# Performance work log

Hardware: AMD Instinct MI355X
Metric: run time of the kernel (lower is better)

Reference implementation:

```python
import jax, jax.numpy as jnp
import numpy as np

B, S, D, NH = 8, 2048, 1024, 8
HD = D // NH          # 128 head dim
UP = 2752             # round_up(2.6667*1024, 64) gated FFN up dim
EPS = 1e-6


def setup_inputs() -> dict:
    key = jax.random.key(0)
    ks = jax.random.split(key, 10)
    s_hd = 1.0 / np.sqrt(HD)
    s_d = 1.0 / np.sqrt(D)
    s_up = 1.0 / np.sqrt(UP)
    return {
        "x": jax.random.normal(ks[0], (B, S, D), jnp.float32),
        "rms1_w": 1.0 + 0.1 * jax.random.normal(ks[1], (D,), jnp.float32),
        "rms2_w": 1.0 + 0.1 * jax.random.normal(ks[2], (D,), jnp.float32),
        # block-diagonal per-head input projections for the 4 gates (i,f,z,o)
        "Wg": jax.random.normal(ks[3], (4, NH, HD, HD), jnp.float32) * s_hd,
        # block-diagonal per-head recurrent weights for the 4 gates
        "R": jax.random.normal(ks[4], (4, NH, HD, HD), jnp.float32) * s_hd,
        "b": jax.random.normal(ks[5], (4, D), jnp.float32) * 0.1,
        "gn_w": 1.0 + 0.1 * jax.random.normal(ks[6], (D,), jnp.float32),
        "W_gate": jax.random.normal(ks[7], (D, UP), jnp.float32) * s_d,
        "W_up": jax.random.normal(ks[8], (D, UP), jnp.float32) * s_d,
        "W_down": jax.random.normal(ks[9], (UP, D), jnp.float32) * s_up,
    }


def _rmsnorm(x, w):
    xf = x.astype(jnp.float32)
    return xf * jax.lax.rsqrt(jnp.mean(xf * xf, axis=-1, keepdims=True) + EPS) * w


def _slstm_block(x, rms1_w, rms2_w, Wg, R, b, gn_w, W_gate, W_up, W_down):
    # --- norm + sLSTM layer ---
    xn = _rmsnorm(x, rms1_w)                     # [B,S,D]
    xh = xn.reshape(B, S, NH, HD)
    # precompute input-side gate preactivations for all timesteps: [S,B,4,NH,HD]
    gx = jnp.einsum('bsni,gnoi->sbgno', xh, Wg) + b.reshape(4, NH, HD)

    zeros = jnp.zeros((B, NH, HD), jnp.float32)
    init = (zeros, zeros, zeros, zeros)          # h, c, n, m

    def step(carry, g):
        h, c, n, m = carry
        pre = g + jnp.einsum('bni,gnoi->bgno', h, R)   # [B,4,NH,HD]
        ir, fr, zr, o_r = pre[:, 0], pre[:, 1], pre[:, 2], pre[:, 3]
        logfplusm = m + jax.nn.log_sigmoid(fr)
        mnew = jnp.maximum(ir, logfplusm)
        i = jnp.exp(ir - mnew)
        f = jnp.exp(logfplusm - mnew)
        cnew = f * c + i * jnp.tanh(zr)
        nnew = f * n + i
        hnew = jax.nn.sigmoid(o_r) * cnew / nnew
        return (hnew, cnew, nnew, mnew), hnew

    (hl, cl, nl, ml), hs = jax.lax.scan(step, init, gx)
    hs = jnp.transpose(hs, (1, 0, 2, 3))         # [B,S,NH,HD]
    # per-head group norm (zero-mean layernorm within each head), weight only
    mu = jnp.mean(hs, axis=-1, keepdims=True)
    var = jnp.var(hs, axis=-1, keepdims=True)
    y = ((hs - mu) * jax.lax.rsqrt(var + EPS)).reshape(B, S, D) * gn_w
    x = x + y                                    # residual
    # --- norm + gated SiLU FFN ---
    xn2 = _rmsnorm(x, rms2_w)
    ff = (jax.nn.silu(xn2 @ W_gate) * (xn2 @ W_up)) @ W_down
    out = x + ff
    state = jnp.stack([hl, cl, nl, ml])          # [4,B,NH,HD] last (h,c,n,m)
    return out, state


def reference(x, rms1_w, rms2_w, Wg, R, b, gn_w, W_gate, W_up, W_down):
    return _slstm_block(x, rms1_w, rms2_w, Wg, R, b, gn_w, W_gate, W_up, W_down)
```

## Files before the change

### kernel.cpp

```cpp
#include <hip/hip_runtime.h>

typedef __bf16 bf16;
typedef bf16 bf16x8 __attribute__((ext_vector_type(8)));
typedef bf16 bf16x4 __attribute__((ext_vector_type(4)));
typedef float f32x4 __attribute__((ext_vector_type(4)));

#define B_ 8
#define S_ 2048
#define D_ 1024
#define NH_ 8
#define HD_ 128
#define UPP 2816
#define ROWS (B_*S_)

__device__ __forceinline__ void gload_lds16(const void* gsrc, void* ldsdst) {
  __builtin_amdgcn_global_load_lds(
      (const __attribute__((address_space(1))) void*)gsrc,
      (__attribute__((address_space(3))) void*)ldsdst, 16, 0, 0);
}

__global__ __launch_bounds__(256) void pack_wgr_kernel(
    const float* __restrict__ Wg, const float* __restrict__ R, const float* __restrict__ bv,
    bf16* __restrict__ Wgpk, bf16* __restrict__ Rpk, float* __restrict__ biaspk)
{
  const float K2 = 1.442695040888963f;
  int idx = blockIdx.x * 256 + threadIdx.x;
  if (idx < 8*512*128) {
    int k = idx & 127, j = (idx >> 7) & 511, n = idx >> 16;
    int g = (j >> 4) & 3, o = ((j >> 6) << 4) | (j & 15);
    float sc = (g == 2) ? 2.f*K2 : K2;
    size_t src = (((size_t)(g*8 + n)*128 + o)*128 + k);
    Wgpk[idx] = (bf16)(Wg[src] * sc);
    Rpk[idx]  = (bf16)(R[src] * sc);
  }
  if (idx < 8*512) {
    int j = idx & 511, n = idx >> 9;
    int g = (j >> 4) & 3, o = ((j >> 6) << 4) | (j & 15);
    float sc = (g == 2) ? 2.f*K2 : K2;
    biaspk[idx] = bv[g*1024 + n*128 + o] * sc;
  }
}

__global__ __launch_bounds__(256) void packT_kernel(
    const float* __restrict__ in, bf16* __restrict__ out,
    int K_out, int N_out, int K_in, int N_in)
{
  __shared__ float tile[64][65];
  int k0 = blockIdx.x * 64, j0 = blockIdx.y * 64;
  int tj = threadIdx.x & 63, t4 = threadIdx.x >> 6;
  #pragma unroll
  for (int p = 0; p < 16; ++p) {
    int kk = p*4 + t4, k = k0 + kk, j = j0 + tj;
    tile[kk][tj] = (k < K_in && j < N_in) ? in[(size_t)k * N_in + j] : 0.f;
  }
  __syncthreads();
  #pragma unroll
  for (int p = 0; p < 16; ++p) {
    int jj = p*4 + t4, j = j0 + jj, k = k0 + tj;
    if (j < N_out && k < K_out) out[(size_t)j * K_out + k] = (bf16)tile[tj][jj];
  }
}

__global__ __launch_bounds__(256) void rmsnorm1_kernel(
    const float* __restrict__ x, const float* __restrict__ w, bf16* __restrict__ xn)
{
  const int row = blockIdx.x, t = threadIdx.x;
  const size_t base = (size_t)row * D_;
  float4 xv = ((const float4*)(x + base))[t];
  float p = xv.x*xv.x + xv.y*xv.y + xv.z*xv.z + xv.w*xv.w;
  #pragma unroll
  for (int m = 1; m <= 32; m <<= 1) p += __shfl_xor(p, m);
  __shared__ float red[4];
  if ((t & 63) == 0) red[t >> 6] = p;
  __syncthreads();
  float rs = rsqrtf((red[0]+red[1]+red[2]+red[3]) * (1.f/1024.f) + 1e-6f);
  float4 wv = ((const float4*)w)[t];
  bf16x4 o;
  o[0] = (bf16)(xv.x*rs*wv.x); o[1] = (bf16)(xv.y*rs*wv.y);
  o[2] = (bf16)(xv.z*rs*wv.z); o[3] = (bf16)(xv.w*rs*wv.w);
  ((bf16x4*)(xn + base))[t] = o;
}

#define BM 128
#define BN 128
#define BKK 64
template<int MODE>
__global__ __launch_bounds__(256) void gemm_bt(
    const bf16* __restrict__ A, int lda,
    const bf16* __restrict__ B, int ldb,
    float* Cf, bf16* Cb, int ldc,
    const float* __restrict__ bias, const float* res, const bf16* gatein, int K)
{
  __shared__ __align__(16) bf16 As[BM*BKK];
  __shared__ __align__(16) bf16 Bs[BN*BKK];
  if constexpr (MODE == 0) {
    const int h = blockIdx.z;
    A += h * HD_;
    B += (size_t)h * (512*128);
    Cb += (size_t)h * ((size_t)ROWS * 512);
    bias += h * 512;
  }
  const int tid = threadIdx.x;
  const int lane = tid & 63, wave = tid >> 6;
  const int row0 = blockIdx.y * BM, col0 = blockIdx.x * BN;
  const int srow = lane >> 3, scol = (lane & 7) * 8;
  const int wr = (wave >> 1) * 64, wc = (wave & 1) * 64;
  const int fr = lane & 15, fg = lane >> 4;
  f32x4 acc[4][4] = {};

  for (int k0 = 0; k0 < K; k0 += BKK) {
    __syncthreads();
    #pragma unroll
    for (int c = 0; c < 4; ++c) {
      const int slot = wave * 4 + c;
      const int r = slot * 8 + srow;
      gload_lds16(A + (size_t)(row0 + r) * lda + (k0 + scol), &As[slot * 512]);
      gload_lds16(B + (size_t)(col0 + r) * ldb + (k0 + scol), &Bs[slot * 512]);
    }
    __syncthreads();
    #pragma unroll
    for (int kk = 0; kk < 2; ++kk) {
      bf16x8 af[4], bfv[4];
      #pragma unroll
      for (int m = 0; m < 4; ++m)
        af[m] = *(const bf16x8*)&As[(wr + m*16 + fr)*BKK + kk*32 + fg*8];
      #pragma unroll
      for (int nn = 0; nn < 4; ++nn)
        bfv[nn] = *(const bf16x8*)&Bs[(wc + nn*16 + fr)*BKK + kk*32 + fg*8];
      #pragma unroll
      for (int m = 0; m < 4; ++m)
        #pragma unroll
        for (int nn = 0; nn < 4; ++nn)
          acc[m][nn] = __builtin_amdgcn_mfma_f32_16x16x32_bf16(af[m], bfv[nn], acc[m][nn], 0, 0, 0);
    }
  }

  #pragma unroll
  for (int m = 0; m < 4; ++m) {
    const int rbase = row0 + wr + m*16 + fg*4;
    #pragma unroll
    for (int nn = 0; nn < 4; ++nn) {
      const int col = col0 + wc + nn*16 + fr;
      #pragma unroll
      for (int j = 0; j < 4; ++j) {
        const size_t off = (size_t)(rbase + j) * ldc + col;
        float v = acc[m][nn][j];
        if constexpr (MODE == 0) Cb[off] = (bf16)(v + bias[col]);
        if constexpr (MODE == 1) Cb[off] = (bf16)v;
        if constexpr (MODE == 2) Cf[off] = v + res[off];
        if constexpr (MODE == 3) {
          float gf = (float)gatein[off];
          Cb[off] = (bf16)(gf / (1.f + __expf(-gf)) * v);
        }
      }
    }
  }
}

__global__ __launch_bounds__(256, 1) void recur_kernel(
    const bf16* __restrict__ gx, const bf16* __restrict__ Rpk,
    bf16* __restrict__ hs, float* __restrict__ stateOut)
{
  const int n  = blockIdx.x >> 2;
  const int bp = blockIdx.x & 3;
  const int tid = threadIdx.x, w = tid >> 6, l = tid & 63;
  const int b16 = l & 15, fg = l >> 4;
  const int bl  = l & 1;
  const int r   = l >> 1;
  const int q   = r >> 4, r16 = r & 15;
  const int b   = bp*2 + bl;
  const int o   = w*32 + r;

  __shared__ __align__(16) bf16 H[2][2][136];
  __shared__ __align__(16) float scr[4][2][8][16];
  for (int i = tid; i < 2*2*136; i += 256) ((bf16*)H)[i] = (bf16)0.f;
  __syncthreads();

  bf16x8 rf[8][4];
  #pragma unroll
  for (int tt = 0; tt < 8; ++tt)
    #pragma unroll
    for (int kk = 0; kk < 4; ++kk)
      rf[tt][kk] = *(const bf16x8*)&Rpk[(size_t)n*65536 + (size_t)(w*128 + tt*16 + b16)*128 + kk*32 + fg*8];

  f32x4 zv = {0.f, 0.f, 0.f, 0.f};
  asm volatile("" : "+v"(zv));

  float cS = 0.f, nS = 0.f, mS = 0.f, hv = 0.f;

  const bf16* gxp = gx + (size_t)n * ROWS * 512 + (size_t)b * S_ * 512
                    + (size_t)(w*2 + q) * 64 + r16;
  bf16* hsp = hs + (size_t)b * S_ * D_ + n * HD_ + o;

  bf16 ga[4][4];
  #pragma unroll
  for (int g = 0; g < 4; ++g) {
    ga[0][g] = gxp[(size_t)0*512 + g*16];
    ga[1][g] = gxp[(size_t)1*512 + g*16];
  }

  auto step = [&](const bf16 (&Hr)[2][136], bf16 (&Hw)[2][136], int s,
                  bf16 (&gU)[4], bf16 (&gF)[4]) {
    bf16x8 hf[4];
    #pragma unroll
    for (int kk = 0; kk < 4; ++kk)
      hf[kk] = *(const bf16x8*)&Hr[b16 & 1][kk*32 + fg*8];

    {
      int sf = (s + 2 < S_) ? s + 2 : 0;
      #pragma unroll
      for (int g = 0; g < 4; ++g)
        gF[g] = gxp[(size_t)sf*512 + g*16];
    }

    f32x4 acc[8];
    #pragma unroll
    for (int tt = 0; tt < 8; ++tt)
      acc[tt] = __builtin_amdgcn_mfma_f32_16x16x32_bf16(rf[tt][0], hf[0], zv, 0, 0, 0);
    #pragma unroll
    for (int kk = 1; kk < 4; ++kk)
      #pragma unroll
      for (int tt = 0; tt < 8; ++tt)
        acc[tt] = __builtin_amdgcn_mfma_f32_16x16x32_bf16(rf[tt][kk], hf[kk], acc[tt], 0, 0, 0);

    if (b16 < 2) {
      #pragma unroll
      for (int tt = 0; tt < 8; ++tt)
        *(f32x4*)&scr[w][b16][tt][fg*4] = acc[tt];
    }
    float pre[4];
    #pragma unroll
    for (int g = 0; g < 4; ++g)
      pre[g] = scr[w][bl][q*4 + g][r16];

    float ir  = pre[0] + (float)gU[0];
    float fr_ = pre[1] + (float)gU[1];
    float zr  = pre[2] + (float)gU[2];
    float og  = pre[3] + (float)gU[3];
    float t   = __builtin_amdgcn_exp2f(-fr_);
    float lfm = mS - __builtin_amdgcn_logf(1.f + t);
    float d   = ir - lfm;
    float e   = __builtin_amdgcn_exp2f(-fabsf(d));
    float iG  = (d >= 0.f) ? 1.f : e;
    float fG  = (d >= 0.f) ? e : 1.f;
    mS = fmaxf(ir, lfm);
    float e2  = __builtin_amdgcn_exp2f(zr);
    float th  = 1.f - 2.f*__builtin_amdgcn_rcpf(e2 + 1.f);
    cS = fG*cS + iG*th;
    nS = fG*nS + iG;
    float eo  = __builtin_amdgcn_exp2f(-og);
    hv = cS * __builtin_amdgcn_rcpf(nS + nS*eo);

    bf16 hb = (bf16)hv;
    Hw[bl][o] = hb;
    hsp[(size_t)s*D_] = hb;

    __builtin_amdgcn_sched_barrier(0);
    __builtin_amdgcn_s_waitcnt(0xC07F);
    __builtin_amdgcn_s_barrier();
    __builtin_amdgcn_sched_barrier(0);
  };

  for (int s = 0; s < S_; s += 4) {
    step(H[0], H[1], s,     ga[0], ga[2]);
    step(H[1], H[0], s + 1, ga[1], ga[3]);
    step(H[0], H[1], s + 2, ga[2], ga[0]);
    step(H[1], H[0], s + 3, ga[3], ga[1]);
  }

  {
    const float LN2 = 0.6931471805599453f;
    size_t sb = ((size_t)b*NH_ + n)*HD_ + o;
    stateOut[sb]         = hv;
    stateOut[8192  + sb] = cS;
    stateOut[16384 + sb] = nS;
    stateOut[24576 + sb] = mS * LN2;
  }
}

__global__ __launch_bounds__(256) void fuse_gn_kernel(
    const bf16* __restrict__ hs, const float* __restrict__ x,
    const float* __restrict__ gnw, const float* __restrict__ r2w,
    float* __restrict__ xr, bf16* __restrict__ xn2)
{
  const int row = blockIdx.x, t = threadIdx.x;
  const size_t base = (size_t)row * D_;
  bf16x4 hraw = ((const bf16x4*)(hs + base))[t];
  float h0 = (float)hraw[0], h1 = (float)hraw[1], h2 = (float)hraw[2], h3 = (float)hraw[3];
  float4 xv = ((const float4*)(x + base))[t];
  float sum = h0 + h1 + h2 + h3;
  float sq  = h0*h0 + h1*h1 + h2*h2 + h3*h3;
  #pragma unroll
  for (int m = 1; m <= 16; m <<= 1) { sum += __shfl_xor(sum, m); sq += __shfl_xor(sq, m); }
  float mu = sum * (1.f/128.f);
  float var = sq * (1.f/128.f) - mu*mu;
  float rstd = rsqrtf(var + 1e-6f);
  float4 gw = ((const float4*)gnw)[t];
  float r0 = xv.x + (h0-mu)*rstd*gw.x;
  float r1 = xv.y + (h1-mu)*rstd*gw.y;
  float r2 = xv.z + (h2-mu)*rstd*gw.z;
  float r3 = xv.w + (h3-mu)*rstd*gw.w;
  ((float4*)(xr + base))[t] = make_float4(r0, r1, r2, r3);
  float p = r0*r0 + r1*r1 + r2*r2 + r3*r3;
  #pragma unroll
  for (int m = 1; m <= 32; m <<= 1) p += __shfl_xor(p, m);
  __shared__ float red[4];
  if ((t & 63) == 0) red[t >> 6] = p;
  __syncthreads();
  float rs = rsqrtf((red[0]+red[1]+red[2]+red[3]) * (1.f/1024.f) + 1e-6f);
  float4 w2 = ((const float4*)r2w)[t];
  bf16x4 o;
  o[0] = (bf16)(r0*rs*w2.x); o[1] = (bf16)(r1*rs*w2.y);
  o[2] = (bf16)(r2*rs*w2.z); o[3] = (bf16)(r3*rs*w2.w);
  ((bf16x4*)(xn2 + base))[t] = o;
}

extern "C" void kernel_launch(void* const* d_in, const int* in_sizes, int n_in,
                              void* d_out, int out_size, void* d_ws, size_t ws_size,
                              hipStream_t stream)
{
  const float* x     = (const float*)d_in[0];
  const float* rms1w = (const float*)d_in[1];
  const float* rms2w = (const float*)d_in[2];
  const float* Wg    = (const float*)d_in[3];
  const float* R     = (const float*)d_in[4];
  const float* bvec  = (const float*)d_in[5];
  const float* gnw   = (const float*)d_in[6];
  const float* Wgate = (const float*)d_in[7];
  const float* Wup   = (const float*)d_in[8];
  const float* Wdown = (const float*)d_in[9];
  float* out = (float*)d_out;
  float* stateOut = out + (size_t)ROWS * D_;

  char* ws = (char*)d_ws;
  size_t off = 0;
  auto alloc = [&](size_t bytes) -> void* {
    void* p = ws + off; off += (bytes + 255) & ~(size_t)255; return p;
  };
  bf16*  xn     = (bf16*)alloc((size_t)ROWS * D_ * 2);
  bf16*  hsbuf  = (bf16*)alloc((size_t)ROWS * D_ * 2);
  bf16*  bigbuf = (bf16*)alloc((size_t)NH_ * ROWS * 512 * 2);
  bf16*  Wgpk   = (bf16*)alloc(8*512*128*2);
  bf16*  Rpk    = (bf16*)alloc(8*512*128*2);
  float* biaspk = (float*)alloc(8*512*4);
  bf16*  Wgatepk = (bf16*)alloc((size_t)UPP * D_ * 2);
  bf16*  Wuppk   = (bf16*)alloc((size_t)UPP * D_ * 2);
  bf16*  Wdownpk = (bf16*)alloc((size_t)D_ * UPP * 2);

  pack_wgr_kernel<<<2048, 256, 0, stream>>>(Wg, R, bvec, Wgpk, Rpk, biaspk);
  packT_kernel<<<dim3(16, 44), 256, 0, stream>>>(Wgate, Wgatepk, 1024, 2816, 1024, 2752);
  packT_kernel<<<dim3(16, 44), 256, 0, stream>>>(Wup,   Wuppk,   1024, 2816, 1024, 2752);
  packT_kernel<<<dim3(44, 16), 256, 0, stream>>>(Wdown, Wdownpk, 2816, 1024, 2752, 1024);

  rmsnorm1_kernel<<<ROWS, 256, 0, stream>>>(x, rms1w, xn);

  gemm_bt<0><<<dim3(4, 128, 8), 256, 0, stream>>>(xn, D_, Wgpk, 128,
      nullptr, bigbuf, 512, biaspk, nullptr, nullptr, 128);

  recur_kernel<<<32, 256, 0, stream>>>(bigbuf, Rpk, hsbuf, stateOut);

  fuse_gn_kernel<<<ROWS, 256, 0, stream>>>(hsbuf, x, gnw, rms2w, out, xn);

  bf16* gate = bigbuf;
  gemm_bt<1><<<dim3(22, 128), 256, 0, stream>>>(xn, D_, Wgatepk, D_,
      nullptr, gate, UPP, nullptr, nullptr, nullptr, D_);
  gemm_bt<3><<<dim3(22, 128), 256, 0, stream>>>(xn, D_, Wuppk, D_,
      nullptr, gate, UPP, nullptr, nullptr, gate, D_);

  gemm_bt<2><<<dim3(8, 128), 256, 0, stream>>>(gate, UPP, Wdownpk, UPP,
      out, nullptr, D_, nullptr, out, nullptr, UPP);
}
```

Baseline: 1.979 ms.

## Split sLSTM recurrence across eight waves per block instead of four

The recurrent kernel now launches 512 threads per block, so each of eight waves computes 16 output units (4 gates x 16 rows) instead of 32. Each wave issues half as many MFMAs per timestep and holds half the recurrent weight registers, which shortens the serial per-step critical path. The trade-off is that only half the lanes do useful elementwise work, and the per-step barrier now has to synchronise eight waves. The scratch layout is padded to 17 floats, likely to reduce LDS bank conflicts.

```diff
diff --git a/kernel.cpp b/kernel.cpp
--- a/kernel.cpp
+++ b/kernel.cpp
@@ -157,7 +157,7 @@
   }
 }
 
-__global__ __launch_bounds__(256, 1) void recur_kernel(
+__global__ __launch_bounds__(512, 1) void recur_kernel(
     const bf16* __restrict__ gx, const bf16* __restrict__ Rpk,
     bf16* __restrict__ hs, float* __restrict__ stateOut)
 {
@@ -166,22 +166,22 @@
   const int tid = threadIdx.x, w = tid >> 6, l = tid & 63;
   const int b16 = l & 15, fg = l >> 4;
   const int bl  = l & 1;
-  const int r   = l >> 1;
-  const int q   = r >> 4, r16 = r & 15;
+  const int r16 = (l >> 1) & 15;
   const int b   = bp*2 + bl;
-  const int o   = w*32 + r;
+  const int o   = w*16 + r16;
+  const bool act = (l < 32);
 
   __shared__ __align__(16) bf16 H[2][2][136];
-  __shared__ __align__(16) float scr[4][2][8][16];
-  for (int i = tid; i < 2*2*136; i += 256) ((bf16*)H)[i] = (bf16)0.f;
+  __shared__ __align__(16) float scr[8][4][2][17];
+  for (int i = tid; i < 2*2*136; i += 512) ((bf16*)H)[i] = (bf16)0.f;
   __syncthreads();
 
-  bf16x8 rf[8][4];
-  #pragma unroll
-  for (int tt = 0; tt < 8; ++tt)
+  bf16x8 rf[4][4];
+  #pragma unroll
+  for (int g = 0; g < 4; ++g)
     #pragma unroll
     for (int kk = 0; kk < 4; ++kk)
-      rf[tt][kk] = *(const bf16x8*)&Rpk[(size_t)n*65536 + (size_t)(w*128 + tt*16 + b16)*128 + kk*32 + fg*8];
+      rf[g][kk] = *(const bf16x8*)&Rpk[(size_t)n*65536 + (size_t)(w*64 + g*16 + b16)*128 + kk*32 + fg*8];
 
   f32x4 zv = {0.f, 0.f, 0.f, 0.f};
   asm volatile("" : "+v"(zv));
@@ -189,7 +189,7 @@
   float cS = 0.f, nS = 0.f, mS = 0.f, hv = 0.f;
 
   const bf16* gxp = gx + (size_t)n * ROWS * 512 + (size_t)b * S_ * 512
-                    + (size_t)(w*2 + q) * 64 + r16;
+                    + (size_t)w * 64 + r16;
   bf16* hsp = hs + (size_t)b * S_ * D_ + n * HD_ + o;
 
   bf16 ga[4][4];
@@ -213,25 +213,25 @@
         gF[g] = gxp[(size_t)sf*512 + g*16];
     }
 
-    f32x4 acc[8];
-    #pragma unroll
-    for (int tt = 0; tt < 8; ++tt)
-      acc[tt] = __builtin_amdgcn_mfma_f32_16x16x32_bf16(rf[tt][0], hf[0], zv, 0, 0, 0);
+    f32x4 acc[4];
+    #pragma unroll
+    for (int g = 0; g < 4; ++g)
+      acc[g] = __builtin_amdgcn_mfma_f32_16x16x32_bf16(rf[g][0], hf[0], zv, 0, 0, 0);
     #pragma unroll
     for (int kk = 1; kk < 4; ++kk)
       #pragma unroll
-      for (int tt = 0; tt < 8; ++tt)
-        acc[tt] = __builtin_amdgcn_mfma_f32_16x16x32_bf16(rf[tt][kk], hf[kk], acc[tt], 0, 0, 0);
+      for (int g = 0; g < 4; ++g)
+        acc[g] = __builtin_amdgcn_mfma_f32_16x16x32_bf16(rf[g][kk], hf[kk], acc[g], 0, 0, 0);
 
     if (b16 < 2) {
       #pragma unroll
-      for (int tt = 0; tt < 8; ++tt)
-        *(f32x4*)&scr[w][b16][tt][fg*4] = acc[tt];
+      for (int g = 0; g < 4; ++g)
+        *(f32x4*)&scr[w][g][b16][fg*4] = acc[g];
     }
     float pre[4];
     #pragma unroll
     for (int g = 0; g < 4; ++g)
-      pre[g] = scr[w][bl][q*4 + g][r16];
+      pre[g] = scr[w][g][bl][r16];
 
     float ir  = pre[0] + (float)gU[0];
     float fr_ = pre[1] + (float)gU[1];
@@ -252,8 +252,10 @@
     hv = cS * __builtin_amdgcn_rcpf(nS + nS*eo);
 
     bf16 hb = (bf16)hv;
-    Hw[bl][o] = hb;
-    hsp[(size_t)s*D_] = hb;
+    if (act) {
+      Hw[bl][o] = hb;
+      hsp[(size_t)s*D_] = hb;
+    }
 
     __builtin_amdgcn_sched_barrier(0);
     __builtin_amdgcn_s_waitcnt(0xC07F);
@@ -268,7 +270,7 @@
     step(H[1], H[0], s + 3, ga[3], ga[1]);
   }
 
-  {
+  if (act) {
     const float LN2 = 0.6931471805599453f;
     size_t sb = ((size_t)b*NH_ + n)*HD_ + o;
     stateOut[sb]         = hv;
@@ -357,7 +359,7 @@
   gemm_bt<0><<<dim3(4, 128, 8), 256, 0, stream>>>(xn, D_, Wgpk, 128,
       nullptr, bigbuf, 512, biaspk, nullptr, nullptr, 128);
 
-  recur_kernel<<<32, 256, 0, stream>>>(bigbuf, Rpk, hsbuf, stateOut);
+  recur_kernel<<<32, 512, 0, stream>>>(bigbuf, Rpk, hsbuf, stateOut);
 
   fuse_gn_kernel<<<ROWS, 256, 0, stream>>>(hsbuf, x, gnw, rms2w, out, xn);
 
```

Result: slower. 2.029 ms (+2.5%).

## Replace FFN GEMMs with 256x256 double-buffered pipelined kernel with swizzled LDS

Applied to the files above, without the earlier changes.

Adds a new gemm256 kernel with 512 threads and 256x256 output tiles for the three FFN matmuls. It double-buffers LDS, overlaps the next k-tile's global-to-LDS loads with MFMA work using explicit waitcnt and barrier phases, XOR-swizzles LDS rows to reduce bank conflicts, and remaps workgroups for better L2 locality. The aim is higher MFMA utilization and less load latency exposure than the old 128x128 single-buffered kernel. The larger tiles mean fewer workgroups (704 or 256), which risks poorer tail balance, and the hand-written wait counts must exactly match the number of outstanding loads.

```diff
diff --git a/kernel.cpp b/kernel.cpp
--- a/kernel.cpp
+++ b/kernel.cpp
@@ -89,10 +89,11 @@
     const bf16* __restrict__ A, int lda,
     const bf16* __restrict__ B, int ldb,
     float* Cf, bf16* Cb, int ldc,
-    const float* __restrict__ bias, const float* res, const bf16* gatein, int K)
+    const float* __restrict__ bias, const float* res, int K)
 {
   __shared__ __align__(16) bf16 As[BM*BKK];
   __shared__ __align__(16) bf16 Bs[BN*BKK];
+  int bx = blockIdx.x, by = blockIdx.y;
   if constexpr (MODE == 0) {
     const int h = blockIdx.z;
     A += h * HD_;
@@ -102,7 +103,7 @@
   }
   const int tid = threadIdx.x;
   const int lane = tid & 63, wave = tid >> 6;
-  const int row0 = blockIdx.y * BM, col0 = blockIdx.x * BN;
+  const int row0 = by * BM, col0 = bx * BN;
   const int srow = lane >> 3, scol = (lane & 7) * 8;
   const int wr = (wave >> 1) * 64, wc = (wave & 1) * 64;
   const int fr = lane & 15, fg = lane >> 4;
@@ -146,12 +147,106 @@
         const size_t off = (size_t)(rbase + j) * ldc + col;
         float v = acc[m][nn][j];
         if constexpr (MODE == 0) Cb[off] = (bf16)(v + bias[col]);
-        if constexpr (MODE == 1) Cb[off] = (bf16)v;
         if constexpr (MODE == 2) Cf[off] = v + res[off];
-        if constexpr (MODE == 3) {
+      }
+    }
+  }
+}
+
+template<int MODE>
+__global__ __launch_bounds__(512, 1) void gemm256(
+    const bf16* __restrict__ A, int lda,
+    const bf16* __restrict__ B, int ldb,
+    float* Cf, bf16* Cb, int ldc,
+    const bf16* gatein, const float* res, int K)
+{
+  __shared__ __align__(16) bf16 As[2][8192];
+  __shared__ __align__(16) bf16 Bs[2][8192];
+  const int gx_ = gridDim.x, nwg = gx_ * gridDim.y;
+  const int wg = blockIdx.y * gx_ + blockIdx.x;
+  const int swzb = (wg & 7) * (nwg >> 3) + (wg >> 3);
+  const int bx = swzb % gx_, by = swzb / gx_;
+  const int row0 = by * 256, col0 = bx * 256;
+  const int tid = threadIdx.x, lane = tid & 63, wave = tid >> 6;
+  const int wm = wave >> 2, wnn = wave & 3;
+  const int fr = lane & 15, fg = lane >> 4;
+  const int srw = lane >> 2, scb = (lane & 3) * 8;
+  const int nt = K >> 5;
+
+  f32x4 acc[8][4] = {};
+
+  auto stage_half = [&](int t, int nbuf, int q) {
+    const bool isA = (q == 0 || q == 3);
+    const int rbase = (q >= 2) ? 128 : 0;
+    const int row = rbase + wave*16 + srw;
+    const int sc = scb ^ (((row >> 3) & 1) << 4);
+    const bf16* src = isA ? (A + (size_t)(row0 + row) * lda + t*32 + sc)
+                          : (B + (size_t)(col0 + row) * ldb + t*32 + sc);
+    bf16* dst = (isA ? As[nbuf] : Bs[nbuf]) + (rbase*32 + wave*512);
+    gload_lds16(src, dst);
+  };
+
+  auto phases = [&](int t, bool st) {
+    const int buf = t & 1;
+    #pragma unroll
+    for (int q = 0; q < 4; ++q) {
+      const int wv = st ? (q < 3 ? 2 : -1)
+                        : (q == 0 ? 2 : q == 1 ? 1 : q == 2 ? 0 : -1);
+      __builtin_amdgcn_sched_barrier(0);
+      if (wv == 2)      asm volatile("s_waitcnt vmcnt(2)");
+      else if (wv == 1) asm volatile("s_waitcnt vmcnt(1)");
+      else if (wv == 0) asm volatile("s_waitcnt vmcnt(0)");
+      __builtin_amdgcn_sched_barrier(0);
+      __builtin_amdgcn_s_barrier();
+      __builtin_amdgcn_sched_barrier(0);
+
+      const int mh = q >> 1, nh = q & 1;
+      bf16x8 af[4], bfv[2];
+      #pragma unroll
+      for (int mm = 0; mm < 4; ++mm) {
+        const int rb = mh*128 + wm*64 + mm*16 + fr;
+        af[mm] = *(const bf16x8*)&As[buf][(rb*32 + fg*8) ^ (((rb >> 3) & 1) << 4)];
+      }
+      #pragma unroll
+      for (int nn = 0; nn < 2; ++nn) {
+        const int rb = nh*128 + wnn*32 + nn*16 + fr;
+        bfv[nn] = *(const bf16x8*)&Bs[buf][(rb*32 + fg*8) ^ (((rb >> 3) & 1) << 4)];
+      }
+      if (st) stage_half(t + 1, buf ^ 1, q);
+      __builtin_amdgcn_s_setprio(1);
+      #pragma unroll
+      for (int mm = 0; mm < 4; ++mm)
+        #pragma unroll
+        for (int nn = 0; nn < 2; ++nn)
+          acc[mh*4+mm][nh*2+nn] = __builtin_amdgcn_mfma_f32_16x16x32_bf16(
+              af[mm], bfv[nn], acc[mh*4+mm][nh*2+nn], 0, 0, 0);
+      __builtin_amdgcn_s_setprio(0);
+      __builtin_amdgcn_sched_barrier(0);
+    }
+  };
+
+  #pragma unroll
+  for (int q = 0; q < 4; ++q) stage_half(0, 0, q);
+
+  for (int t = 0; t < nt - 1; ++t) phases(t, true);
+  phases(nt - 1, false);
+
+  #pragma unroll
+  for (int m = 0; m < 8; ++m) {
+    const int grow = row0 + (m>>2)*128 + wm*64 + (m&3)*16 + fg*4;
+    #pragma unroll
+    for (int n = 0; n < 4; ++n) {
+      const int gcol = col0 + (n>>1)*128 + wnn*32 + (n&1)*16 + fr;
+      #pragma unroll
+      for (int jj = 0; jj < 4; ++jj) {
+        const size_t off = (size_t)(grow + jj) * ldc + gcol;
+        float v = acc[m][n][jj];
+        if constexpr (MODE == 0) Cb[off] = (bf16)v;
+        if constexpr (MODE == 1) {
           float gf = (float)gatein[off];
           Cb[off] = (bf16)(gf / (1.f + __expf(-gf)) * v);
         }
+        if constexpr (MODE == 2) Cf[off] = v + res[off];
       }
     }
   }
@@ -355,18 +450,17 @@
   rmsnorm1_kernel<<<ROWS, 256, 0, stream>>>(x, rms1w, xn);
 
   gemm_bt<0><<<dim3(4, 128, 8), 256, 0, stream>>>(xn, D_, Wgpk, 128,
-      nullptr, bigbuf, 512, biaspk, nullptr, nullptr, 128);
+      nullptr, bigbuf, 512, biaspk, nullptr, 128);
 
   recur_kernel<<<32, 256, 0, stream>>>(bigbuf, Rpk, hsbuf, stateOut);
 
   fuse_gn_kernel<<<ROWS, 256, 0, stream>>>(hsbuf, x, gnw, rms2w, out, xn);
 
   bf16* gate = bigbuf;
-  gemm_bt<1><<<dim3(22, 128), 256, 0, stream>>>(xn, D_, Wgatepk, D_,
-      nullptr, gate, UPP, nullptr, nullptr, nullptr, D_);
-  gemm_bt<3><<<dim3(22, 128), 256, 0, stream>>>(xn, D_, Wuppk, D_,
-      nullptr, gate, UPP, nullptr, nullptr, gate, D_);
-
-  gemm_bt<2><<<dim3(8, 128), 256, 0, stream>>>(gate, UPP, Wdownpk, UPP,
-      out, nullptr, D_, nullptr, out, nullptr, UPP);
-}
+  gemm256<0><<<dim3(11, 64), 512, 0, stream>>>(xn, D_, Wgatepk, D_,
+      nullptr, gate, UPP, nullptr, nullptr, D_);
+  gemm256<1><<<dim3(11, 64), 512, 0, stream>>>(xn, D_, Wuppk, D_,
+      nullptr, gate, UPP, gate, nullptr, D_);
+  gemm256<2><<<dim3(4, 64), 512, 0, stream>>>(gate, UPP, Wdownpk, UPP,
+      out, nullptr, D_, nullptr, out, UPP);
+}
```

Measured after the change: 1.988 ms. No clear change (+0.4%).
